# Performance work log

Hardware: AMD Instinct MI355X
Metric: run time of the kernel (lower is better)

Reference implementation:

```python
import jax, jax.numpy as jnp
import numpy as np

T = 8192
INPUT = 1024
TRACE = 64
CTX = 16
OUT = 1024
EPS = 1e-5  # equinox LayerNorm default


def _linear(key, out_f, in_f):
    k1, k2 = jax.random.split(key)
    lim = 1.0 / np.sqrt(in_f)
    w = jax.random.uniform(k1, (out_f, in_f), minval=-lim, maxval=lim, dtype=jnp.float32)
    b = jax.random.uniform(k2, (out_f,), minval=-lim, maxval=lim, dtype=jnp.float32)
    return w, b


def setup_inputs() -> dict:
    key = jax.random.key(0)
    ks = jax.random.split(key, 8)
    x = jax.random.normal(ks[0], (T, INPUT), dtype=jnp.float32)
    start = jax.random.randint(ks[1], (T,), 0, 2).astype(bool)
    next_done = jax.random.randint(ks[2], (T,), 0, 2).astype(bool)
    state_re = jnp.zeros((1, TRACE, CTX), dtype=jnp.float32)
    state_im = jnp.zeros((1, TRACE, CTX), dtype=jnp.float32)
    pre_w, pre_b = _linear(ks[3], TRACE, INPUT)
    gi_w, gi_b = _linear(ks[4], TRACE, INPUT)
    go_w, go_b = _linear(ks[5], OUT, INPUT)
    skip_w, skip_b = _linear(ks[6], OUT, INPUT)
    mix_w, mix_b = _linear(ks[7], OUT, 2 * TRACE * CTX)
    # ffa.init: deterministic decay rates a and oscillation freqs b
    ffa_a = jnp.linspace(1e-6, 0.5, TRACE, dtype=jnp.float32)
    ffa_b = (2.0 * jnp.pi / jnp.exp(jnp.linspace(jnp.log(1.0), jnp.log(1024.0), CTX))).astype(jnp.float32)
    return dict(x=x, state_re=state_re, state_im=state_im, start=start, next_done=next_done,
                pre_w=pre_w, pre_b=pre_b, gi_w=gi_w, gi_b=gi_b, go_w=go_w, go_b=go_b,
                skip_w=skip_w, skip_b=skip_b, mix_w=mix_w, mix_b=mix_b,
                ffa_a=ffa_a, ffa_b=ffa_b)


def _ffa_apply(ffa_a, ffa_b, gated_x, state0, start):
    """Resettable complex linear recurrence: s_t = gamma * s_{t-1} + x_t, reset at episode starts.
    gamma = exp(-|a| + i b), outer over (trace, context). Parallelized with an associative scan
    over monoid elements (reset_flag, state, elapsed_steps)."""
    Tn, m = gated_x.shape
    c = ffa_b.shape[0]
    ab = jax.lax.complex(
        jnp.broadcast_to(-jnp.abs(ffa_a)[None, :, None], (1, m, c)),
        jnp.broadcast_to(ffa_b[None, None, :], (1, m, c)),
    )  # [1, m, c] complex: log-gamma per unit timestep

    xc = jnp.broadcast_to(gated_x[:, :, None].astype(jnp.complex64), (Tn, m, c))
    # prepend carried-in recurrent state: timestep 0, no reset
    x_e = jnp.concatenate([state0.astype(jnp.complex64), xc], axis=0)          # [T+1, m, c]
    s_e = jnp.concatenate([jnp.zeros((1, 1, 1), bool), start[:, None, None]], axis=0)
    i_e = jnp.concatenate([jnp.zeros((1, 1, 1), jnp.float32),
                           jnp.ones((Tn, 1, 1), jnp.float32)], axis=0)

    def op(a, b):
        s1, x1, i1 = a
        s2, x2, i2 = b
        # zero the carried state across episode boundaries
        x1 = jnp.where(s2, 0.0, x1)
        i1 = jnp.where(s2, 0.0, i1)
        g = jnp.exp(ab * i2.astype(jnp.complex64))  # decay over i2 elapsed steps
        return (jnp.logical_or(s1, s2), x1 * g + x2, i1 + i2)

    _, states, _ = jax.lax.associative_scan(op, (s_e, x_e, i_e), axis=0)
    return states[1:]  # [T, m, c] complex64


def reference(x, state_re, state_im, start, next_done,
              pre_w, pre_b, gi_w, gi_b, go_w, go_b,
              skip_w, skip_b, mix_w, mix_b, ffa_a, ffa_b):
    gate_in = jax.nn.sigmoid(x @ gi_w.T + gi_b)          # [T, trace]
    pre = x @ pre_w.T + pre_b                            # [T, trace]
    gated_x = pre * gate_in

    state0 = jax.lax.complex(state_re, state_im)         # [1, trace, ctx]
    state = _ffa_apply(ffa_a, ffa_b, gated_x, state0, start)  # [T, trace, ctx] complex

    z_in = jnp.concatenate([jnp.real(state), jnp.imag(state)], axis=-1)
    z_in = z_in.reshape(state.shape[0], -1)              # [T, 2*trace*ctx]
    z = z_in @ mix_w.T + mix_b                           # [T, out]

    gate_out = jax.nn.sigmoid(x @ go_w.T + go_b)         # [T, out]
    skip = x @ skip_w.T + skip_b                         # [T, out]

    zg = z * gate_out
    mu = zg.mean(-1, keepdims=True)
    var = ((zg - mu) ** 2).mean(-1, keepdims=True)
    ln = (zg - mu) / jnp.sqrt(var + EPS)                 # LayerNorm, no affine

    out = ln + skip * (1.0 - gate_out)
    final_state = state[-1:]
    return out, final_state


if __name__ == "__main__":
    inp = setup_inputs()
    out, fs = jax.jit(reference)(**inp)
    print(out.shape, out.dtype, fs.shape, fs.dtype)
```

## Files before the change

### kernel.cpp

```cpp
#include <hip/hip_runtime.h>
#include <math.h>

#define T_DIM 8192
#define IN_DIM 1024
#define TRACE 64
#define CTX 16
#define OUT_DIM 1024
#define KMIX 2048

typedef __attribute__((ext_vector_type(8))) short bf16x8;
typedef __attribute__((ext_vector_type(4))) float f32x4;
typedef __attribute__((ext_vector_type(16))) float f32x16;

__device__ __forceinline__ unsigned short f2bf(float f) {
    unsigned int u = __float_as_uint(f);
    u = (u + 0x7FFFu + ((u >> 16) & 1u)) >> 16;
    return (unsigned short)u;
}
__device__ __forceinline__ float bf2f(unsigned short b) {
    return __uint_as_float(((unsigned int)b) << 16);
}

__device__ __forceinline__ void gl2lds16(const void* g, void* l) {
    __builtin_amdgcn_global_load_lds(
        (const __attribute__((address_space(1))) unsigned int*)g,
        (__attribute__((address_space(3))) unsigned int*)l,
        16, 0, 0);
}


__global__ __launch_bounds__(256) void c0_conv(const float* __restrict__ x,
        const float* __restrict__ gw, const float* __restrict__ sw, const float* __restrict__ mw,
        const float* __restrict__ pw, const float* __restrict__ giw,
        const void* __restrict__ startp,
        unsigned short* __restrict__ xb, unsigned short* __restrict__ gob,
        unsigned short* __restrict__ skb, unsigned short* __restrict__ mixb,
        unsigned short* __restrict__ pwb, unsigned short* __restrict__ gwb,
        unsigned char* __restrict__ mask)
{
    if (blockIdx.x == 0) {
        __shared__ int nonbool;
        int tid = threadIdx.x;
        if (tid == 0) nonbool = 0;
        __syncthreads();
        const unsigned int* wv = (const unsigned int*)startp;
        #pragma unroll
        for (int p = 0; p < 8; p++) {
            unsigned int a = wv[tid * 8 + p];
            if (a > 1u) nonbool = 1;
        }
        __syncthreads();
        if (nonbool) {
            const unsigned char* s8 = (const unsigned char*)startp;
            for (int i = tid; i < T_DIM; i += 256) mask[i] = (unsigned char)(s8[i] != 0);
        } else {
            const int* s32 = (const int*)startp;
            for (int i = tid; i < T_DIM; i += 256) mask[i] = (unsigned char)(s32[i] != 0);
        }
    }
    const size_t QX = 2097152, QG = 262144, QS = 262144, QM = 524288, QP = 16384, QI = 16384;
    const size_t total = QX + QG + QS + QM + QP + QI;
    for (size_t q = (size_t)blockIdx.x * blockDim.x + threadIdx.x; q < total;
         q += (size_t)gridDim.x * blockDim.x) {
        const float* src; unsigned short* dst; size_t i;
        if (q < QX)                  { src = x;   dst = xb;   i = q; }
        else if (q < QX+QG)          { src = gw;  dst = gob;  i = q - QX; }
        else if (q < QX+QG+QS)       { src = sw;  dst = skb;  i = q - QX - QG; }
        else if (q < QX+QG+QS+QM)    { src = mw;  dst = mixb; i = q - QX - QG - QS; }
        else if (q < QX+QG+QS+QM+QP) { src = pw;  dst = pwb;  i = q - QX - QG - QS - QM; }
        else                         { src = giw; dst = gwb;  i = q - QX - QG - QS - QM - QP; }
        float4 v = *(const float4*)(src + i * 4);
        ushort4 o;
        o.x = f2bf(v.x); o.y = f2bf(v.y); o.z = f2bf(v.z); o.w = f2bf(v.w);
        *(ushort4*)(dst + i * 4) = o;
    }
}

__global__ __launch_bounds__(256) void k1_mfma(const unsigned short* __restrict__ xb,
        const unsigned short* __restrict__ pwb, const unsigned short* __restrict__ gwb,
        const float* __restrict__ pre_b, const float* __restrict__ gi_b,
        float* __restrict__ gxT)
{
    __shared__ __align__(16) unsigned short As[1024];
    __shared__ __align__(16) unsigned short Bs[4096];
    __shared__ float sgE[64][33];

    const int tid = threadIdx.x;
    const int t0 = blockIdx.x * 32;
    const int lane = tid & 63, w = tid >> 6;
    const int quad = lane >> 4, l16 = lane & 15;
    const int r = tid >> 2, s4 = tid & 3;
    const int csw = (s4 - ((r >> 1) & 3)) & 3;

    f32x4 acc[2][2];
    const f32x4 zero4 = {0.f, 0.f, 0.f, 0.f};
    #pragma unroll
    for (int mi = 0; mi < 2; mi++)
        #pragma unroll
        for (int ni = 0; ni < 2; ni++) acc[mi][ni] = zero4;

    const int sfr = (quad + ((l16 >> 1) & 3)) & 3;

    for (int k0 = 0; k0 < IN_DIM; k0 += 32) {
        __syncthreads();
        if (tid < 128) {
            int ra = tid >> 2;
            int ca = ((tid & 3) - ((ra >> 1) & 3)) & 3;
            gl2lds16(xb + (size_t)(t0 + ra) * IN_DIM + k0 + ca * 8, As + tid * 8);
        }
        gl2lds16(pwb + (size_t)r * IN_DIM + k0 + csw * 8, Bs + tid * 8);
        gl2lds16(gwb + (size_t)r * IN_DIM + k0 + csw * 8, Bs + 2048 + tid * 8);
        asm volatile("s_waitcnt vmcnt(0)" ::: "memory");
        __syncthreads();
        bf16x8 af[2], bf[2];
        #pragma unroll
        for (int mi = 0; mi < 2; mi++)
            af[mi] = *(const bf16x8*)&As[(mi * 16 + l16) * 32 + sfr * 8];
        #pragma unroll
        for (int ni = 0; ni < 2; ni++)
            bf[ni] = *(const bf16x8*)&Bs[(w * 32 + ni * 16 + l16) * 32 + sfr * 8];
        #pragma unroll
        for (int mi = 0; mi < 2; mi++)
            #pragma unroll
            for (int ni = 0; ni < 2; ni++)
                acc[mi][ni] = __builtin_amdgcn_mfma_f32_16x16x32_bf16(af[mi], bf[ni], acc[mi][ni], 0, 0, 0);
    }

    if (w >= 2) {
        #pragma unroll
        for (int mi = 0; mi < 2; mi++)
            #pragma unroll
            for (int ni = 0; ni < 2; ni++) {
                int mg = (w - 2) * 32 + ni * 16 + l16;
                float gb = gi_b[mg];
                #pragma unroll
                for (int rr = 0; rr < 4; rr++) {
                    int tl = mi * 16 + quad * 4 + rr;
                    sgE[mg][tl] = 1.f / (1.f + expf(-(acc[mi][ni][rr] + gb)));
                }
            }
    }
    __syncthreads();
    if (w < 2) {
        #pragma unroll
        for (int mi = 0; mi < 2; mi++)
            #pragma unroll
            for (int ni = 0; ni < 2; ni++) {
                int mp = w * 32 + ni * 16 + l16;
                float pb = pre_b[mp];
                float4 o;
                float* po = &o.x;
                #pragma unroll
                for (int rr = 0; rr < 4; rr++) {
                    int tl = mi * 16 + quad * 4 + rr;
                    po[rr] = (acc[mi][ni][rr] + pb) * sgE[mp][tl];
                }
                *(float4*)&gxT[(size_t)mp * T_DIM + t0 + mi * 16 + quad * 4] = o;
            }
    }
}

__global__ __launch_bounds__(128) void k2_scan(const float* __restrict__ gxT,
        const unsigned char* __restrict__ mask8,
        const float* __restrict__ state_re, const float* __restrict__ state_im,
        const float* __restrict__ ffa_a, const float* __restrict__ ffa_b,
        unsigned short* __restrict__ zinTb, float* __restrict__ fstate)
{
    const int m = blockIdx.x >> 4;
    const int c = blockIdx.x & 15;
    const int j = threadIdx.x;
    __shared__ float Br[128], Bi[128], Er[128], Ei[128];
    __shared__ unsigned char Rf[128];
    __shared__ unsigned int SB[128 * 33];

    const float am = -fabsf(ffa_a[m]);
    const float bc = ffa_b[c];
    const float er = expf(am);
    const float gr = er * cosf(bc);
    const float gi = er * sinf(bc);

    const float* gx = gxT + (size_t)m * T_DIM;
    const int t0 = j * 64;

    unsigned long long rmask = 0ull;
    float sre = 0.f, sim = 0.f;
    bool r = false;
    #pragma unroll 8
    for (int i = 0; i < 64; i++) {
        int t = t0 + i;
        if (mask8[t]) { rmask |= 1ull << i; sre = 0.f; sim = 0.f; r = true; }
        else { float tr_ = sre * gr - sim * gi; sim = sre * gi + sim * gr; sre = tr_; }
        sre += gx[t];
    }
    Br[j] = sre; Bi[j] = sim; Rf[j] = r ? 1 : 0;
    __syncthreads();
    if (j == 0) {
        float e64  = expf(64.f * am);
        float g64r = e64 * cosf(64.f * bc);
        float g64i = e64 * sinf(64.f * bc);
        float pr = state_re[m * CTX + c], pi = state_im[m * CTX + c];
        for (int q = 0; q < 128; q++) {
            Er[q] = pr; Ei[q] = pi;
            if (Rf[q]) { pr = Br[q]; pi = Bi[q]; }
            else {
                float nr = pr * g64r - pi * g64i + Br[q];
                pi       = pr * g64i + pi * g64r + Bi[q];
                pr = nr;
            }
        }
    }
    __syncthreads();
    sre = Er[j]; sim = Ei[j];
    unsigned int ore[32], oim[32];
    #pragma unroll
    for (int i = 0; i < 64; i++) {
        int t = t0 + i;
        if (rmask & (1ull << i)) { sre = 0.f; sim = 0.f; }
        else { float tr_ = sre * gr - sim * gi; sim = sre * gi + sim * gr; sre = tr_; }
        sre += gx[t];
        unsigned short hr = f2bf(sre), hi_ = f2bf(sim);
        if (i & 1) { ore[i >> 1] |= ((unsigned int)hr) << 16; oim[i >> 1] |= ((unsigned int)hi_) << 16; }
        else       { ore[i >> 1]  = hr;                        oim[i >> 1]  = hi_; }
    }
    if (j == 127) {
        int p = m * CTX + c;
        fstate[p]        = sre;
        fstate[1024 + p] = sim;
    }

    unsigned short* zreb = zinTb + (size_t)(m * 32 + c)      * T_DIM;
    unsigned short* zimb = zinTb + (size_t)(m * 32 + 16 + c) * T_DIM;

    #pragma unroll
    for (int q = 0; q < 32; q++) SB[j * 33 + q] = ore[q];
    __syncthreads();
    #pragma unroll
    for (int it = 0; it < 8; it++) {
        int g = (it * 128 + j) * 4;
        int jj = g >> 5, qq = g & 31;
        uint4 v = *(uint4*)&SB[jj * 33 + qq];
        *(uint4*)(zreb + g * 2) = v;
    }
    __syncthreads();
    #pragma unroll
    for (int q = 0; q < 32; q++) SB[j * 33 + q] = oim[q];
    __syncthreads();
    #pragma unroll
    for (int it = 0; it < 8; it++) {
        int g = (it * 128 + j) * 4;
        int jj = g >> 5, qq = g & 31;
        uint4 v = *(uint4*)&SB[jj * 33 + qq];
        *(uint4*)(zimb + g * 2) = v;
    }
}

__global__ __launch_bounds__(256) void t3_tr(const unsigned short* __restrict__ zinTb,
                                             unsigned short* __restrict__ zinb)
{
    __shared__ unsigned short S[64][72];
    const int k0 = blockIdx.x * 64, t0 = blockIdx.y * 64;
    const int tid = threadIdx.x;
    {
        int kr = tid >> 3, tc = (tid & 7) * 8;
        #pragma unroll
        for (int p = 0; p < 2; p++) {
            int k = kr + p * 32;
            ushort4 a = *(const ushort4*)&zinTb[(size_t)(k0 + k) * T_DIM + t0 + tc];
            ushort4 b = *(const ushort4*)&zinTb[(size_t)(k0 + k) * T_DIM + t0 + tc + 4];
            *(ushort4*)&S[k][tc]     = a;
            *(ushort4*)&S[k][tc + 4] = b;
        }
    }
    __syncthreads();
    {
        int tr = tid >> 3, kc = (tid & 7) * 8;
        #pragma unroll
        for (int p = 0; p < 2; p++) {
            int t = tr + p * 32;
            ushort4 o1, o2;
            o1.x = S[kc+0][t]; o1.y = S[kc+1][t]; o1.z = S[kc+2][t]; o1.w = S[kc+3][t];
            o2.x = S[kc+4][t]; o2.y = S[kc+5][t]; o2.z = S[kc+6][t]; o2.w = S[kc+7][t];
            *(ushort4*)&zinb[(size_t)(t0 + t) * KMIX + k0 + kc]     = o1;
            *(ushort4*)&zinb[(size_t)(t0 + t) * KMIX + k0 + kc + 4] = o2;
        }
    }
}

__global__ __launch_bounds__(256, 2) void gA_gemm(
        const unsigned short* __restrict__ xb,   const unsigned short* __restrict__ zinb,
        const unsigned short* __restrict__ gob,  const unsigned short* __restrict__ skb,
        const unsigned short* __restrict__ mixb,
        const float* __restrict__ go_b, const float* __restrict__ skip_b, const float* __restrict__ mix_b,
        unsigned short* __restrict__ zg, unsigned short* __restrict__ sk2)
{
    __shared__ __align__(16) unsigned short As[8192];
    __shared__ __align__(16) unsigned short Bs[8192];
    __shared__ __align__(16) unsigned short Cs[8192];
    const int tid = threadIdx.x;
    const int b = blockIdx.x;
    const int xcd = b & 7, q = b >> 3;
    const int t0 = (xcd * 8 + (q >> 3)) * 128;
    const int n0 = (q & 7) * 128;

    const int lane = tid & 63, w = tid >> 6;
    const int wm = w >> 1, wn = w & 1;
    const int l31 = lane & 31, h = lane >> 5;
    const int r = tid >> 2;
    const int csw = ((tid & 3) - ((r >> 1) & 3)) & 3;
    const int c8 = csw * 8;
    const int srot = (l31 >> 1) & 3;

    f32x16 accg[2][2], acck[2][2];
    #pragma unroll
    for (int mi = 0; mi < 2; mi++)
        #pragma unroll
        for (int ni = 0; ni < 2; ni++)
            #pragma unroll
            for (int e = 0; e < 16; e++) { accg[mi][ni][e] = 0.f; acck[mi][ni][e] = 0.f; }

    {
        const unsigned short* gA0 = xb  + (size_t)(t0 + r)      * IN_DIM + c8;
        const unsigned short* gA1 = xb  + (size_t)(t0 + 64 + r) * IN_DIM + c8;
        const unsigned short* gB0 = gob + (size_t)(n0 + r)      * IN_DIM + c8;
        const unsigned short* gB1 = gob + (size_t)(n0 + 64 + r) * IN_DIM + c8;
        const unsigned short* gC0 = skb + (size_t)(n0 + r)      * IN_DIM + c8;
        const unsigned short* gC1 = skb + (size_t)(n0 + 64 + r) * IN_DIM + c8;
        for (int k0 = 0; k0 < IN_DIM; k0 += 64) {
            __syncthreads();
            gl2lds16(gA0 + k0,      As + tid * 8);
            gl2lds16(gA1 + k0,      As + 2048 + tid * 8);
            gl2lds16(gA0 + k0 + 32, As + 4096 + tid * 8);
            gl2lds16(gA1 + k0 + 32, As + 6144 + tid * 8);
            gl2lds16(gB0 + k0,      Bs + tid * 8);
            gl2lds16(gB1 + k0,      Bs + 2048 + tid * 8);
            gl2lds16(gB0 + k0 + 32, Bs + 4096 + tid * 8);
            gl2lds16(gB1 + k0 + 32, Bs + 6144 + tid * 8);
            gl2lds16(gC0 + k0,      Cs + tid * 8);
            gl2lds16(gC1 + k0,      Cs + 2048 + tid * 8);
            gl2lds16(gC0 + k0 + 32, Cs + 4096 + tid * 8);
            gl2lds16(gC1 + k0 + 32, Cs + 6144 + tid * 8);
            asm volatile("s_waitcnt vmcnt(0)" ::: "memory");
            __syncthreads();
            #pragma unroll
            for (int kq = 0; kq < 4; kq++) {
                const int sub = kq >> 1, kh = kq & 1;
                const int sfr = ((kh * 2 + h) + srot) & 3;
                const int sb4 = sub * 4096 + sfr * 8;
                bf16x8 af[2], bg[2], bk[2];
                #pragma unroll
                for (int mi = 0; mi < 2; mi++)
                    af[mi] = *(const bf16x8*)&As[sb4 + (wm * 64 + mi * 32 + l31) * 32];
                #pragma unroll
                for (int ni = 0; ni < 2; ni++) {
                    bg[ni] = *(const bf16x8*)&Bs[sb4 + (wn * 64 + ni * 32 + l31) * 32];
                    bk[ni] = *(const bf16x8*)&Cs[sb4 + (wn * 64 + ni * 32 + l31) * 32];
                }
                #pragma unroll
                for (int mi = 0; mi < 2; mi++)
                    #pragma unroll
                    for (int ni = 0; ni < 2; ni++) {
                        accg[mi][ni] = __builtin_amdgcn_mfma_f32_32x32x16_bf16(af[mi], bg[ni], accg[mi][ni], 0, 0, 0);
                        acck[mi][ni] = __builtin_amdgcn_mfma_f32_32x32x16_bf16(af[mi], bk[ni], acck[mi][ni], 0, 0, 0);
                    }
            }
        }
    }

    unsigned int sigp[32];
    #pragma unroll
    for (int mi = 0; mi < 2; mi++)
        #pragma unroll
        for (int ni = 0; ni < 2; ni++) {
            int n = n0 + wn * 64 + ni * 32 + l31;
            float gb = go_b[n];
            float sb_ = skip_b[n];
            #pragma unroll
            for (int reg = 0; reg < 16; reg++) {
                int row = (reg & 3) + 8 * (reg >> 2) + 4 * h;
                int t = t0 + wm * 64 + mi * 32 + row;
                float s = 1.f / (1.f + expf(-(accg[mi][ni][reg] + gb)));
                sk2[(size_t)t * OUT_DIM + n] = f2bf((acck[mi][ni][reg] + sb_) * (1.f - s));
                unsigned int pk = (unsigned int)f2bf(s);
                int idx = (mi * 2 + ni) * 8 + (reg >> 1);
                if (reg & 1) sigp[idx] |= pk << 16;
                else         sigp[idx]  = pk;
            }
        }

    #pragma unroll
    for (int mi = 0; mi < 2; mi++)
        #pragma unroll
        for (int ni = 0; ni < 2; ni++)
            #pragma unroll
            for (int e = 0; e < 16; e++) accg[mi][ni][e] = 0.f;
    {
        const unsigned short* gA0 = zinb + (size_t)(t0 + r)      * KMIX + c8;
        const unsigned short* gA1 = zinb + (size_t)(t0 + 64 + r) * KMIX + c8;
        const unsigned short* gB0 = mixb + (size_t)(n0 + r)      * KMIX + c8;
        const unsigned short* gB1 = mixb + (size_t)(n0 + 64 + r) * KMIX + c8;
        for (int k0 = 0; k0 < KMIX; k0 += 64) {
            __syncthreads();
            gl2lds16(gA0 + k0,      As + tid * 8);
            gl2lds16(gA1 + k0,      As + 2048 + tid * 8);
            gl2lds16(gA0 + k0 + 32, As + 4096 + tid * 8);
            gl2lds16(gA1 + k0 + 32, As + 6144 + tid * 8);
            gl2lds16(gB0 + k0,      Bs + tid * 8);
            gl2lds16(gB1 + k0,      Bs + 2048 + tid * 8);
            gl2lds16(gB0 + k0 + 32, Bs + 4096 + tid * 8);
            gl2lds16(gB1 + k0 + 32, Bs + 6144 + tid * 8);
            asm volatile("s_waitcnt vmcnt(0)" ::: "memory");
            __syncthreads();
            #pragma unroll
            for (int kq = 0; kq < 4; kq++) {
                const int sub = kq >> 1, kh = kq & 1;
                const int sfr = ((kh * 2 + h) + srot) & 3;
                const int sb4 = sub * 4096 + sfr * 8;
                bf16x8 af[2], bf[2];
                #pragma unroll
                for (int mi = 0; mi < 2; mi++)
                    af[mi] = *(const bf16x8*)&As[sb4 + (wm * 64 + mi * 32 + l31) * 32];
                #pragma unroll
                for (int ni = 0; ni < 2; ni++)
                    bf[ni] = *(const bf16x8*)&Bs[sb4 + (wn * 64 + ni * 32 + l31) * 32];
                #pragma unroll
                for (int mi = 0; mi < 2; mi++)
                    #pragma unroll
                    for (int ni = 0; ni < 2; ni++)
                        accg[mi][ni] = __builtin_amdgcn_mfma_f32_32x32x16_bf16(af[mi], bf[ni], accg[mi][ni], 0, 0, 0);
            }
        }
    }

    #pragma unroll
    for (int mi = 0; mi < 2; mi++)
        #pragma unroll
        for (int ni = 0; ni < 2; ni++) {
            int n = n0 + wn * 64 + ni * 32 + l31;
            float mb_ = mix_b[n];
            #pragma unroll
            for (int reg = 0; reg < 16; reg++) {
                int row = (reg & 3) + 8 * (reg >> 2) + 4 * h;
                int t = t0 + wm * 64 + mi * 32 + row;
                unsigned int u = sigp[(mi * 2 + ni) * 8 + (reg >> 1)];
                float sig = bf2f((unsigned short)((reg & 1) ? (u >> 16) : (u & 0xffff)));
                zg[(size_t)t * OUT_DIM + n] = f2bf((accg[mi][ni][reg] + mb_) * sig);
            }
        }
}

__global__ __launch_bounds__(256) void g3_ln(const unsigned short* __restrict__ zg,
        const unsigned short* __restrict__ sk2, float* __restrict__ out)
{
    __shared__ float sb[4], qb[4];
    __shared__ float mu_s, rstd_s;
    const int t = blockIdx.x;
    const int tid = threadIdx.x;
    ushort4 zu = *(const ushort4*)&zg [(size_t)t * OUT_DIM + tid * 4];
    ushort4 su = *(const ushort4*)&sk2[(size_t)t * OUT_DIM + tid * 4];
    float z0 = bf2f(zu.x), z1 = bf2f(zu.y), z2 = bf2f(zu.z), z3 = bf2f(zu.w);
    float s0 = bf2f(su.x), s1 = bf2f(su.y), s2 = bf2f(su.z), s3 = bf2f(su.w);
    float s = z0 + z1 + z2 + z3;
    float q = z0*z0 + z1*z1 + z2*z2 + z3*z3;
    #pragma unroll
    for (int off = 32; off > 0; off >>= 1) {
        s += __shfl_down(s, off, 64);
        q += __shfl_down(q, off, 64);
    }
    int wid = tid >> 6;
    if ((tid & 63) == 0) { sb[wid] = s; qb[wid] = q; }
    __syncthreads();
    if (tid == 0) {
        float S = sb[0] + sb[1] + sb[2] + sb[3];
        float Q = qb[0] + qb[1] + qb[2] + qb[3];
        float mu = S * (1.f / 1024.f);
        float var = Q * (1.f / 1024.f) - mu * mu;
        mu_s = mu; rstd_s = rsqrtf(var + 1e-5f);
    }
    __syncthreads();
    float mu = mu_s, rs = rstd_s;
    float4 o;
    o.x = (z0 - mu) * rs + s0;
    o.y = (z1 - mu) * rs + s1;
    o.z = (z2 - mu) * rs + s2;
    o.w = (z3 - mu) * rs + s3;
    *(float4*)&out[(size_t)t * OUT_DIM + tid * 4] = o;
}

__global__ void g4_final(const float* __restrict__ fstate, float* __restrict__ out, int out_size)
{
    int i = blockIdx.x * blockDim.x + threadIdx.x;
    if (i >= 2048) return;
    long long base = (long long)T_DIM * OUT_DIM;
    if (base + i < (long long)out_size) out[base + i] = fstate[i];
}

extern "C" void kernel_launch(void* const* d_in, const int* in_sizes, int n_in,
                              void* d_out, int out_size, void* d_ws, size_t ws_size,
                              hipStream_t stream) {
    const float* x        = (const float*)d_in[0];
    const float* state_re = (const float*)d_in[1];
    const float* state_im = (const float*)d_in[2];
    const void*  startp   = d_in[3];
    const float* pre_w    = (const float*)d_in[5];
    const float* pre_b    = (const float*)d_in[6];
    const float* gi_w     = (const float*)d_in[7];
    const float* gi_b     = (const float*)d_in[8];
    const float* go_w     = (const float*)d_in[9];
    const float* go_b     = (const float*)d_in[10];
    const float* skip_w   = (const float*)d_in[11];
    const float* skip_b   = (const float*)d_in[12];
    const float* mix_w    = (const float*)d_in[13];
    const float* mix_b    = (const float*)d_in[14];
    const float* ffa_a    = (const float*)d_in[15];
    const float* ffa_b    = (const float*)d_in[16];

    float* ws = (float*)d_ws;
    float*          gxT    = ws;
    unsigned short* zinTb  = (unsigned short*)(ws + 524288);
    unsigned short* zinb   = (unsigned short*)(ws + 8912896);
    unsigned short* xb     = (unsigned short*)(ws + 17301504);
    unsigned short* gob    = (unsigned short*)(ws + 21495808);
    unsigned short* skb    = (unsigned short*)(ws + 22020096);
    unsigned short* mixb   = (unsigned short*)(ws + 22544384);
    unsigned short* zg     = (unsigned short*)(ws + 23592960);
    unsigned short* sk2    = (unsigned short*)(ws + 27787264);
    float*          fstate = ws + 31981568;
    unsigned char*  mask   = (unsigned char*)(ws + 31983616);
    unsigned short* pwb    = zg;
    unsigned short* gwb    = zg + 65536;
    float* out = (float*)d_out;

    hipLaunchKernelGGL(c0_conv,  dim3(1536),    dim3(256),  0, stream, x, go_w, skip_w, mix_w, pre_w, gi_w,
                                                             startp, xb, gob, skb, mixb, pwb, gwb, mask);
    hipLaunchKernelGGL(k1_mfma,  dim3(256),     dim3(256),  0, stream, xb, pwb, gwb, pre_b, gi_b, gxT);
    hipLaunchKernelGGL(k2_scan,  dim3(1024),    dim3(128),  0, stream, gxT, mask, state_re, state_im, ffa_a, ffa_b, zinTb, fstate);
    hipLaunchKernelGGL(t3_tr,    dim3(32, 128), dim3(256),  0, stream, zinTb, zinb);
    hipLaunchKernelGGL(gA_gemm,  dim3(512),     dim3(256),  0, stream, xb, zinb, gob, skb, mixb, go_b, skip_b, mix_b, zg, sk2);
    hipLaunchKernelGGL(g3_ln,    dim3(8192),    dim3(256),  0, stream, zg, sk2, out);
    hipLaunchKernelGGL(g4_final, dim3(8),       dim3(256),  0, stream, fstate, out, out_size);
}
```

Measured before the change: 293.7 us.

## Triple-buffer gA_gemm LDS pipeline with 512-thread 256x128 tiles

Rewrites the fused gate/skip and mix GEMM kernel to use 512-thread blocks covering 256 rows by 128 columns, halving the grid to 256 blocks. The K loop now uses a three-stage LDS ring of 32-wide K slices, issuing async global-to-LDS loads two steps ahead with partial vmcnt waits instead of a full drain and double barrier per step. It also raises wave priority around the MFMA bursts. This aims to hide global load latency and cut synchronization stalls. The cost is 96KB of LDS per block, which likely limits occupancy to one block per CU, and fewer blocks than the CU count.

```diff
diff --git a/kernel.cpp b/kernel.cpp
--- a/kernel.cpp
+++ b/kernel.cpp
@@ -286,20 +286,18 @@
     }
 }
 
-__global__ __launch_bounds__(256, 2) void gA_gemm(
+__global__ __launch_bounds__(512, 2) void gA_gemm(
         const unsigned short* __restrict__ xb,   const unsigned short* __restrict__ zinb,
         const unsigned short* __restrict__ gob,  const unsigned short* __restrict__ skb,
         const unsigned short* __restrict__ mixb,
         const float* __restrict__ go_b, const float* __restrict__ skip_b, const float* __restrict__ mix_b,
         unsigned short* __restrict__ zg, unsigned short* __restrict__ sk2)
 {
-    __shared__ __align__(16) unsigned short As[8192];
-    __shared__ __align__(16) unsigned short Bs[8192];
-    __shared__ __align__(16) unsigned short Cs[8192];
+    __shared__ __align__(16) unsigned short L[49152];
     const int tid = threadIdx.x;
     const int b = blockIdx.x;
     const int xcd = b & 7, q = b >> 3;
-    const int t0 = (xcd * 8 + (q >> 3)) * 128;
+    const int t0 = (xcd * 4 + (q >> 3)) * 256;
     const int n0 = (q & 7) * 128;
 
     const int lane = tid & 63, w = tid >> 6;
@@ -309,6 +307,7 @@
     const int csw = ((tid & 3) - ((r >> 1) & 3)) & 3;
     const int c8 = csw * 8;
     const int srot = (l31 >> 1) & 3;
+    const int dst8 = tid * 8;
 
     f32x16 accg[2][2], acck[2][2];
     #pragma unroll
@@ -319,42 +318,44 @@
             for (int e = 0; e < 16; e++) { accg[mi][ni][e] = 0.f; acck[mi][ni][e] = 0.f; }
 
     {
-        const unsigned short* gA0 = xb  + (size_t)(t0 + r)      * IN_DIM + c8;
-        const unsigned short* gA1 = xb  + (size_t)(t0 + 64 + r) * IN_DIM + c8;
-        const unsigned short* gB0 = gob + (size_t)(n0 + r)      * IN_DIM + c8;
-        const unsigned short* gB1 = gob + (size_t)(n0 + 64 + r) * IN_DIM + c8;
-        const unsigned short* gC0 = skb + (size_t)(n0 + r)      * IN_DIM + c8;
-        const unsigned short* gC1 = skb + (size_t)(n0 + 64 + r) * IN_DIM + c8;
-        for (int k0 = 0; k0 < IN_DIM; k0 += 64) {
-            __syncthreads();
-            gl2lds16(gA0 + k0,      As + tid * 8);
-            gl2lds16(gA1 + k0,      As + 2048 + tid * 8);
-            gl2lds16(gA0 + k0 + 32, As + 4096 + tid * 8);
-            gl2lds16(gA1 + k0 + 32, As + 6144 + tid * 8);
-            gl2lds16(gB0 + k0,      Bs + tid * 8);
-            gl2lds16(gB1 + k0,      Bs + 2048 + tid * 8);
-            gl2lds16(gB0 + k0 + 32, Bs + 4096 + tid * 8);
-            gl2lds16(gB1 + k0 + 32, Bs + 6144 + tid * 8);
-            gl2lds16(gC0 + k0,      Cs + tid * 8);
-            gl2lds16(gC1 + k0,      Cs + 2048 + tid * 8);
-            gl2lds16(gC0 + k0 + 32, Cs + 4096 + tid * 8);
-            gl2lds16(gC1 + k0 + 32, Cs + 6144 + tid * 8);
-            asm volatile("s_waitcnt vmcnt(0)" ::: "memory");
-            __syncthreads();
-            #pragma unroll
-            for (int kq = 0; kq < 4; kq++) {
-                const int sub = kq >> 1, kh = kq & 1;
-                const int sfr = ((kh * 2 + h) + srot) & 3;
-                const int sb4 = sub * 4096 + sfr * 8;
+        const unsigned short* gA0 = xb  + (size_t)(t0 + r)       * IN_DIM + c8;
+        const unsigned short* gA1 = xb  + (size_t)(t0 + 128 + r) * IN_DIM + c8;
+        const unsigned short* gB0 = gob + (size_t)(n0 + r)       * IN_DIM + c8;
+        const unsigned short* gC0 = skb + (size_t)(n0 + r)       * IN_DIM + c8;
+
+#define STAGE_F(bufi, kof) do {                         \
+        unsigned short* _b = &L[(bufi) * 16384];        \
+        gl2lds16(gA0 + (kof), _b + dst8);               \
+        gl2lds16(gA1 + (kof), _b + 4096 + dst8);        \
+        gl2lds16(gB0 + (kof), _b + 8192 + dst8);        \
+        gl2lds16(gC0 + (kof), _b + 12288 + dst8);       \
+    } while (0)
+
+        STAGE_F(0, 0);
+        STAGE_F(1, 32);
+        asm volatile("s_waitcnt vmcnt(4)" ::: "memory");
+        __builtin_amdgcn_s_barrier();
+
+        int cur = 0, nx2 = 2;
+        for (int t = 0; t < 32; ++t) {
+            const unsigned short* As = &L[cur * 16384];
+            const unsigned short* Bs = As + 8192;
+            const unsigned short* Cs = As + 12288;
+            const bool st = (t + 2 < 32);
+            #pragma unroll
+            for (int kh = 0; kh < 2; kh++) {
+                const int so = ((kh * 2 + h + srot) & 3) * 8;
                 bf16x8 af[2], bg[2], bk[2];
                 #pragma unroll
                 for (int mi = 0; mi < 2; mi++)
-                    af[mi] = *(const bf16x8*)&As[sb4 + (wm * 64 + mi * 32 + l31) * 32];
+                    af[mi] = *(const bf16x8*)&As[(wm * 64 + mi * 32 + l31) * 32 + so];
                 #pragma unroll
                 for (int ni = 0; ni < 2; ni++) {
-                    bg[ni] = *(const bf16x8*)&Bs[sb4 + (wn * 64 + ni * 32 + l31) * 32];
-                    bk[ni] = *(const bf16x8*)&Cs[sb4 + (wn * 64 + ni * 32 + l31) * 32];
+                    bg[ni] = *(const bf16x8*)&Bs[(wn * 64 + ni * 32 + l31) * 32 + so];
+                    bk[ni] = *(const bf16x8*)&Cs[(wn * 64 + ni * 32 + l31) * 32 + so];
                 }
+                if (kh == 0 && st) STAGE_F(nx2, (t + 2) * 32);
+                __builtin_amdgcn_s_setprio(1);
                 #pragma unroll
                 for (int mi = 0; mi < 2; mi++)
                     #pragma unroll
@@ -362,8 +363,15 @@
                         accg[mi][ni] = __builtin_amdgcn_mfma_f32_32x32x16_bf16(af[mi], bg[ni], accg[mi][ni], 0, 0, 0);
                         acck[mi][ni] = __builtin_amdgcn_mfma_f32_32x32x16_bf16(af[mi], bk[ni], acck[mi][ni], 0, 0, 0);
                     }
-            }
-        }
+                __builtin_amdgcn_s_setprio(0);
+            }
+            if (st) { asm volatile("s_waitcnt vmcnt(4)" ::: "memory"); }
+            else    { asm volatile("s_waitcnt vmcnt(0)" ::: "memory"); }
+            __builtin_amdgcn_s_barrier();
+            cur = (cur == 2) ? 0 : cur + 1;
+            nx2 = (nx2 == 2) ? 0 : nx2 + 1;
+        }
+#undef STAGE_F
     }
 
     unsigned int sigp[32];
@@ -394,41 +402,53 @@
             #pragma unroll
             for (int e = 0; e < 16; e++) accg[mi][ni][e] = 0.f;
     {
-        const unsigned short* gA0 = zinb + (size_t)(t0 + r)      * KMIX + c8;
-        const unsigned short* gA1 = zinb + (size_t)(t0 + 64 + r) * KMIX + c8;
-        const unsigned short* gB0 = mixb + (size_t)(n0 + r)      * KMIX + c8;
-        const unsigned short* gB1 = mixb + (size_t)(n0 + 64 + r) * KMIX + c8;
-        for (int k0 = 0; k0 < KMIX; k0 += 64) {
-            __syncthreads();
-            gl2lds16(gA0 + k0,      As + tid * 8);
-            gl2lds16(gA1 + k0,      As + 2048 + tid * 8);
-            gl2lds16(gA0 + k0 + 32, As + 4096 + tid * 8);
-            gl2lds16(gA1 + k0 + 32, As + 6144 + tid * 8);
-            gl2lds16(gB0 + k0,      Bs + tid * 8);
-            gl2lds16(gB1 + k0,      Bs + 2048 + tid * 8);
-            gl2lds16(gB0 + k0 + 32, Bs + 4096 + tid * 8);
-            gl2lds16(gB1 + k0 + 32, Bs + 6144 + tid * 8);
-            asm volatile("s_waitcnt vmcnt(0)" ::: "memory");
-            __syncthreads();
-            #pragma unroll
-            for (int kq = 0; kq < 4; kq++) {
-                const int sub = kq >> 1, kh = kq & 1;
-                const int sfr = ((kh * 2 + h) + srot) & 3;
-                const int sb4 = sub * 4096 + sfr * 8;
+        const unsigned short* mA0 = zinb + (size_t)(t0 + r)       * KMIX + c8;
+        const unsigned short* mA1 = zinb + (size_t)(t0 + 128 + r) * KMIX + c8;
+        const unsigned short* mB0 = mixb + (size_t)(n0 + r)       * KMIX + c8;
+
+#define STAGE_M(bufi, kof) do {                         \
+        unsigned short* _b = &L[(bufi) * 16384];        \
+        gl2lds16(mA0 + (kof), _b + dst8);               \
+        gl2lds16(mA1 + (kof), _b + 4096 + dst8);        \
+        gl2lds16(mB0 + (kof), _b + 8192 + dst8);        \
+    } while (0)
+
+        STAGE_M(0, 0);
+        STAGE_M(1, 32);
+        asm volatile("s_waitcnt vmcnt(3)" ::: "memory");
+        __builtin_amdgcn_s_barrier();
+
+        int cur = 0, nx2 = 2;
+        for (int t = 0; t < 64; ++t) {
+            const unsigned short* As = &L[cur * 16384];
+            const unsigned short* Bs = As + 8192;
+            const bool st = (t + 2 < 64);
+            #pragma unroll
+            for (int kh = 0; kh < 2; kh++) {
+                const int so = ((kh * 2 + h + srot) & 3) * 8;
                 bf16x8 af[2], bf[2];
                 #pragma unroll
                 for (int mi = 0; mi < 2; mi++)
-                    af[mi] = *(const bf16x8*)&As[sb4 + (wm * 64 + mi * 32 + l31) * 32];
+                    af[mi] = *(const bf16x8*)&As[(wm * 64 + mi * 32 + l31) * 32 + so];
                 #pragma unroll
                 for (int ni = 0; ni < 2; ni++)
-                    bf[ni] = *(const bf16x8*)&Bs[sb4 + (wn * 64 + ni * 32 + l31) * 32];
+                    bf[ni] = *(const bf16x8*)&Bs[(wn * 64 + ni * 32 + l31) * 32 + so];
+                if (kh == 0 && st) STAGE_M(nx2, (t + 2) * 32);
+                __builtin_amdgcn_s_setprio(1);
                 #pragma unroll
                 for (int mi = 0; mi < 2; mi++)
                     #pragma unroll
                     for (int ni = 0; ni < 2; ni++)
                         accg[mi][ni] = __builtin_amdgcn_mfma_f32_32x32x16_bf16(af[mi], bf[ni], accg[mi][ni], 0, 0, 0);
-            }
-        }
+                __builtin_amdgcn_s_setprio(0);
+            }
+            if (st) { asm volatile("s_waitcnt vmcnt(3)" ::: "memory"); }
+            else    { asm volatile("s_waitcnt vmcnt(0)" ::: "memory"); }
+            __builtin_amdgcn_s_barrier();
+            cur = (cur == 2) ? 0 : cur + 1;
+            nx2 = (nx2 == 2) ? 0 : nx2 + 1;
+        }
+#undef STAGE_M
     }
 
     #pragma unroll
@@ -535,7 +555,7 @@
     hipLaunchKernelGGL(k1_mfma,  dim3(256),     dim3(256),  0, stream, xb, pwb, gwb, pre_b, gi_b, gxT);
     hipLaunchKernelGGL(k2_scan,  dim3(1024),    dim3(128),  0, stream, gxT, mask, state_re, state_im, ffa_a, ffa_b, zinTb, fstate);
     hipLaunchKernelGGL(t3_tr,    dim3(32, 128), dim3(256),  0, stream, zinTb, zinb);
-    hipLaunchKernelGGL(gA_gemm,  dim3(512),     dim3(256),  0, stream, xb, zinb, gob, skb, mixb, go_b, skip_b, mix_b, zg, sk2);
+    hipLaunchKernelGGL(gA_gemm,  dim3(256),     dim3(512),  0, stream, xb, zinb, gob, skb, mixb, go_b, skip_b, mix_b, zg, sk2);
     hipLaunchKernelGGL(g3_ln,    dim3(8192),    dim3(256),  0, stream, zg, sk2, out);
     hipLaunchKernelGGL(g4_final, dim3(8),       dim3(256),  0, stream, fstate, out, out_size);
 }
```

Measured after the change: 296.9 us. No clear change (+1.1%).
